# Optimization experiments

Measured on AMD Instinct MI355X. Metric: run time of the kernel, lower is better.

The kernel has to match this reference:

```python
import jax, jax.numpy as jnp
import numpy as np

B, N, D, H = 2, 2048, 1024, 8
HD = D // H  # head_dim = 128
EPS = 1e-6


def setup_inputs() -> dict:
    key = jax.random.key(0)
    ks = jax.random.split(key, 11)
    std = 0.02
    w = lambda k, shape: jax.random.normal(k, shape, dtype=jnp.float32) * std
    return {
        "x": jax.random.normal(ks[0], (B, N, D), dtype=jnp.float32),
        "Wq": w(ks[1], (D, D)),
        "Wk": w(ks[2], (D, D)),
        "Wv": w(ks[3], (D, D)),
        "Wf1": w(ks[4], (D, HD)),
        "Wf2": w(ks[5], (HD, D)),
        "Wbeta": w(ks[6], (D, H)),
        "Wog1": w(ks[7], (D, HD)),
        "Wog2": w(ks[8], (HD, D)),
        "norm_w": jnp.ones((D,), dtype=jnp.float32),
        "Wo": w(ks[9], (D, D)),
    }


def _interleave(a, b):
    # [B,T,H,HD] x2 -> [B,2T,H,HD], order a0,b0,a1,b1,...  (rearrange 'b (c n) -> b (n c)', c=2)
    return jnp.stack([a, b], axis=2).reshape(a.shape[0], 2 * a.shape[1], a.shape[2], a.shape[3])


def _l2norm(x):
    return x / jnp.sqrt(jnp.sum(x * x, axis=-1, keepdims=True) + EPS)


def _dense_rnn(x, Wq, Wk, Wv, Wf1, Wf2, Wbeta, Wog1, Wog2, norm_w, Wo):
    b, n, d = x.shape
    q = jax.nn.silu(x @ Wq)
    k = jax.nn.silu(x @ Wk)
    v = jax.nn.silu(x @ Wv)
    f = (x @ Wf1) @ Wf2                       # low-rank f_proj
    log_f = jax.nn.log_sigmoid(f)
    beta = jax.nn.sigmoid(x @ Wbeta) * 2.0    # [B,N,H], beta_activation='neg'

    shp = (b, n, H, HD)
    q, k, v, log_f = (t.reshape(shp) for t in (q, k, v, log_f))
    k = _l2norm(k)
    k_ = -beta[..., None] * k                 # k * -beta
    zero = jnp.zeros(shp, x.dtype)

    # DPLR doubling: per token, step0 = gated decay + Diag(f)*k k^T, step1 = (I-kk^T)S + k v^T
    gk = _interleave(log_f, zero)
    a = _interleave(k_ * jnp.exp(log_f), k_)
    bb = _interleave(k, k)
    kk = _interleave(zero, k)
    vv = _interleave(zero, v)
    qq = _interleave(zero, q)

    seq = tuple(jnp.moveaxis(t, 1, 0) for t in (gk, a, bb, kk, vv, qq))  # time-major [2N,B,H,HD]
    S0 = jnp.zeros((b, H, HD, HD), x.dtype)

    def step(S, inp):
        g, a_t, b_t, k_t, v_t, q_t = inp
        # S_t = Diag(exp(g)) S + a (b^T S) + k v^T  ; o_t = q^T S_t
        bS = jnp.einsum('bhk,bhkv->bhv', b_t, S)
        S = jnp.exp(g)[..., None] * S + a_t[..., None] * bS[:, :, None, :] + k_t[..., None] * v_t[:, :, None, :]
        o = jnp.einsum('bhk,bhkv->bhv', q_t, S)
        return S, o

    _, o = jax.lax.scan(step, S0, seq)        # o: [2N,B,H,HD]
    o = jnp.moveaxis(o, 0, 1)[:, 1::2]        # take update-step outputs (last n after de-interleave)
    out = o.reshape(b, n, d)

    # gated rmsnorm (gate_pos='pre', sigmoid gate, group = per head) then o_proj
    gate = (x @ Wog1) @ Wog2
    y = out * jax.nn.sigmoid(gate)
    yh = y.reshape(b, n, H, HD)
    yh = yh / jnp.sqrt(jnp.mean(yh * yh, axis=-1, keepdims=True) + EPS)
    y = yh.reshape(b, n, d) * norm_w
    return y @ Wo


def reference(x, Wq, Wk, Wv, Wf1, Wf2, Wbeta, Wog1, Wog2, norm_w, Wo):
    return _dense_rnn(x, Wq, Wk, Wv, Wf1, Wf2, Wbeta, Wog1, Wog2, norm_w, Wo)
```

## Files before the change

### kernel.cpp

```cpp
#include <hip/hip_runtime.h>
#include <cmath>


#define SZT ((size_t)4096 * 1024)
#define RECF 520
#define RECSTRIDE 4160
#define TOKB 16
#define SLOTB 1600

typedef unsigned short u16;
typedef __attribute__((ext_vector_type(8))) short short8;
typedef __attribute__((ext_vector_type(4))) float f32x4;

__device__ __forceinline__ float sigmf(float x) { return 1.f / (1.f + expf(-x)); }
__device__ __forceinline__ float siluf(float x) { return x * sigmf(x); }
__device__ __forceinline__ u16 f2bf(float f) {
    unsigned int u = __float_as_uint(f);
    unsigned int r = (u + 0x7FFFu + ((u >> 16) & 1u)) >> 16;
    return (u16)r;
}
__device__ __forceinline__ float bf2f(u16 h) { return __uint_as_float((unsigned int)h << 16); }
__device__ __forceinline__ void splitbf(float f, u16& hi, u16& lo) {
    hi = f2bf(f);
    lo = f2bf(f - bf2f(hi));
}

#define GLOAD_LDS16(gp, lp) __builtin_amdgcn_global_load_lds( \
    (const __attribute__((address_space(1))) void*)(gp),      \
    (__attribute__((address_space(3))) void*)(lp), 16, 0, 0)

__global__ __launch_bounds__(256) void wtrans_split_g(
    const float* __restrict__ W, u16* __restrict__ WTh, u16* __restrict__ WTl,
    int K, int N)
{
    __shared__ float t[32][33];
    const int tx = threadIdx.x & 31, ty = threadIdx.x >> 5;
    const int n0 = blockIdx.x * 32, k0 = blockIdx.y * 32;
#pragma unroll
    for (int i = 0; i < 4; i++)
        t[ty + i * 8][tx] = W[(size_t)(k0 + ty + i * 8) * N + n0 + tx];
    __syncthreads();
#pragma unroll
    for (int i = 0; i < 4; i++) {
        u16 hi, lo;
        splitbf(t[tx][ty + i * 8], hi, lo);
        WTh[(size_t)(n0 + ty + i * 8) * K + k0 + tx] = hi;
        WTl[(size_t)(n0 + ty + i * 8) * K + k0 + tx] = lo;
    }
}

__global__ __launch_bounds__(256) void wtrans(const float* __restrict__ W, u16* __restrict__ WT)
{
    __shared__ float t[32][33];
    const int tx = threadIdx.x & 31, ty = threadIdx.x >> 5;
    const int n0 = blockIdx.x * 32, k0 = blockIdx.y * 32;
#pragma unroll
    for (int i = 0; i < 4; i++)
        t[ty + i * 8][tx] = W[(size_t)(k0 + ty + i * 8) * 1024 + n0 + tx];
    __syncthreads();
#pragma unroll
    for (int i = 0; i < 4; i++)
        WT[(size_t)(n0 + ty + i * 8) * 1024 + k0 + tx] = f2bf(t[tx][ty + i * 8]);
}

__global__ __launch_bounds__(256) void conv_split(
    const float* __restrict__ in, u16* __restrict__ oh, u16* __restrict__ ol)
{
    const size_t i = ((size_t)blockIdx.x * 256 + threadIdx.x) * 8;
    short8 rh, rl;
#pragma unroll
    for (int j = 0; j < 8; j++) {
        u16 hi, lo;
        splitbf(in[i + j], hi, lo);
        rh[j] = (short)hi; rl[j] = (short)lo;
    }
    *(short8*)&oh[i] = rh;
    *(short8*)&ol[i] = rl;
}

__global__ __launch_bounds__(256) void wcat_kernel(
    const float* __restrict__ Wf1, const float* __restrict__ Wog1, float* __restrict__ Wcat)
{
    const int idx = blockIdx.x * 256 + threadIdx.x;
    const int k = idx >> 8, j = idx & 255;
    Wcat[idx] = (j < 128) ? Wf1[k * 128 + j] : Wog1[k * 128 + j - 128];
}

__global__ __launch_bounds__(256) void beta_kernel(
    const float* __restrict__ x, const float* __restrict__ Wbeta, float* __restrict__ beta)
{
    const int row = blockIdx.x;
    const int tid = threadIdx.x;
    const int lane = tid & 63, wid = tid >> 6;
    __shared__ float wsum[4][8];
    float4 xv = *(const float4*)&x[(size_t)row * 1024 + tid * 4];
    float p[8];
#pragma unroll
    for (int h = 0; h < 8; h++)
        p[h] = xv.x * Wbeta[(size_t)(tid * 4 + 0) * 8 + h]
             + xv.y * Wbeta[(size_t)(tid * 4 + 1) * 8 + h]
             + xv.z * Wbeta[(size_t)(tid * 4 + 2) * 8 + h]
             + xv.w * Wbeta[(size_t)(tid * 4 + 3) * 8 + h];
#pragma unroll
    for (int off = 32; off >= 1; off >>= 1)
#pragma unroll
        for (int h = 0; h < 8; h++) p[h] += __shfl_xor(p[h], off);
    if (lane == 0)
#pragma unroll
        for (int h = 0; h < 8; h++) wsum[wid][h] = p[h];
    __syncthreads();
    if (tid < 8) {
        float s = wsum[0][tid] + wsum[1][tid] + wsum[2][tid] + wsum[3][tid];
        beta[(size_t)row * 8 + tid] = 2.f * sigmf(s);
    }
}

__global__ __launch_bounds__(256) void gemm_bf16_split(
    const u16* __restrict__ Ah, const u16* __restrict__ Al,
    const u16* __restrict__ BTh, const u16* __restrict__ BTl,
    float* __restrict__ C, int M, int N, int K, int lda, int ldb)
{
    __shared__ u16 AsH[128 * 32];
    __shared__ u16 AsL[128 * 32];
    __shared__ u16 BsH[128 * 32];
    __shared__ u16 BsL[128 * 32];
    const int tid = threadIdx.x;
    const int lane = tid & 63;
    const int w = tid >> 6;
    const int wr = w >> 1, wc = w & 1;
    const int row0 = blockIdx.y * 128;
    const int col0 = blockIdx.x * 128;
    const int mrow = lane & 15;
    const int kgrp = (lane >> 4) * 8;

    f32x4 acc[4][4] = {};

    const int off0 = w * 1024 + lane * 16;
    const int r0 = off0 >> 6, kl0 = (off0 & 63) >> 1;
    const int off1 = off0 + 4096;
    const int r1 = off1 >> 6, kl1 = (off1 & 63) >> 1;

    for (int kt = 0; kt < K; kt += 32) {
        GLOAD_LDS16(Ah  + (size_t)(row0 + r0) * lda + kt + kl0, (char*)AsH + w * 1024);
        GLOAD_LDS16(Ah  + (size_t)(row0 + r1) * lda + kt + kl1, (char*)AsH + w * 1024 + 4096);
        GLOAD_LDS16(Al  + (size_t)(row0 + r0) * lda + kt + kl0, (char*)AsL + w * 1024);
        GLOAD_LDS16(Al  + (size_t)(row0 + r1) * lda + kt + kl1, (char*)AsL + w * 1024 + 4096);
        GLOAD_LDS16(BTh + (size_t)(col0 + r0) * ldb + kt + kl0, (char*)BsH + w * 1024);
        GLOAD_LDS16(BTh + (size_t)(col0 + r1) * ldb + kt + kl1, (char*)BsH + w * 1024 + 4096);
        GLOAD_LDS16(BTl + (size_t)(col0 + r0) * ldb + kt + kl0, (char*)BsL + w * 1024);
        GLOAD_LDS16(BTl + (size_t)(col0 + r1) * ldb + kt + kl1, (char*)BsL + w * 1024 + 4096);
        __syncthreads();

        short8 aH[4], aL[4], bH[4], bL[4];
#pragma unroll
        for (int mi = 0; mi < 4; ++mi) {
            aH[mi] = *(const short8*)&AsH[(wr * 64 + mi * 16 + mrow) * 32 + kgrp];
            aL[mi] = *(const short8*)&AsL[(wr * 64 + mi * 16 + mrow) * 32 + kgrp];
        }
#pragma unroll
        for (int ni = 0; ni < 4; ++ni) {
            bH[ni] = *(const short8*)&BsH[(wc * 64 + ni * 16 + mrow) * 32 + kgrp];
            bL[ni] = *(const short8*)&BsL[(wc * 64 + ni * 16 + mrow) * 32 + kgrp];
        }
#pragma unroll
        for (int mi = 0; mi < 4; ++mi)
#pragma unroll
            for (int ni = 0; ni < 4; ++ni) {
                acc[mi][ni] = __builtin_amdgcn_mfma_f32_16x16x32_bf16(aH[mi], bH[ni], acc[mi][ni], 0, 0, 0);
                acc[mi][ni] = __builtin_amdgcn_mfma_f32_16x16x32_bf16(aL[mi], bH[ni], acc[mi][ni], 0, 0, 0);
                acc[mi][ni] = __builtin_amdgcn_mfma_f32_16x16x32_bf16(aH[mi], bL[ni], acc[mi][ni], 0, 0, 0);
            }
        __syncthreads();
    }

    const int crow = (lane >> 4) * 4;
#pragma unroll
    for (int mi = 0; mi < 4; ++mi)
#pragma unroll
        for (int ni = 0; ni < 4; ++ni)
#pragma unroll
            for (int j = 0; j < 4; ++j)
                C[(size_t)(row0 + wr * 64 + mi * 16 + crow + j) * N + col0 + wc * 64 + ni * 16 + mrow]
                    = acc[mi][ni][j];
}

__global__ __launch_bounds__(256) void corr_gemm(
    const u16* __restrict__ Ah, const u16* __restrict__ Al,
    const u16* __restrict__ BTh, const u16* __restrict__ BTl,
    float* __restrict__ OV)
{
    __shared__ u16 AsH[128 * 32];
    __shared__ u16 AsL[128 * 32];
    __shared__ u16 BsH[128 * 32];
    __shared__ u16 BsL[128 * 32];
    const int tid = threadIdx.x;
    const int lane = tid & 63;
    const int w = tid >> 6;
    const int wr = w >> 1, wc = w & 1;
    const int row0 = blockIdx.y * 128;
    const int mrow = lane & 15;
    const int kgrp = (lane >> 4) * 8;

    const int bh = blockIdx.z;
    const int b = bh >> 3, h = bh & 7;
    const size_t aoff = (size_t)b * 2097152 + (size_t)h * 128;
    const size_t boff = (size_t)bh * 16384;
    const size_t coff = (size_t)b * 2097152 + (size_t)1048576 + (size_t)h * 128;

    f32x4 acc[4][4] = {};

    const int off0 = w * 1024 + lane * 16;
    const int r0 = off0 >> 6, kl0 = (off0 & 63) >> 1;
    const int off1 = off0 + 4096;
    const int r1 = off1 >> 6, kl1 = (off1 & 63) >> 1;

    for (int kt = 0; kt < 128; kt += 32) {
        GLOAD_LDS16(Ah  + aoff + (size_t)(row0 + r0) * 1024 + kt + kl0, (char*)AsH + w * 1024);
        GLOAD_LDS16(Ah  + aoff + (size_t)(row0 + r1) * 1024 + kt + kl1, (char*)AsH + w * 1024 + 4096);
        GLOAD_LDS16(Al  + aoff + (size_t)(row0 + r0) * 1024 + kt + kl0, (char*)AsL + w * 1024);
        GLOAD_LDS16(Al  + aoff + (size_t)(row0 + r1) * 1024 + kt + kl1, (char*)AsL + w * 1024 + 4096);
        GLOAD_LDS16(BTh + boff + (size_t)r0 * 128 + kt + kl0, (char*)BsH + w * 1024);
        GLOAD_LDS16(BTh + boff + (size_t)r1 * 128 + kt + kl1, (char*)BsH + w * 1024 + 4096);
        GLOAD_LDS16(BTl + boff + (size_t)r0 * 128 + kt + kl0, (char*)BsL + w * 1024);
        GLOAD_LDS16(BTl + boff + (size_t)r1 * 128 + kt + kl1, (char*)BsL + w * 1024 + 4096);
        __syncthreads();

        short8 aH[4], aL[4], bH[4], bL[4];
#pragma unroll
        for (int mi = 0; mi < 4; ++mi) {
            aH[mi] = *(const short8*)&AsH[(wr * 64 + mi * 16 + mrow) * 32 + kgrp];
            aL[mi] = *(const short8*)&AsL[(wr * 64 + mi * 16 + mrow) * 32 + kgrp];
        }
#pragma unroll
        for (int ni = 0; ni < 4; ++ni) {
            bH[ni] = *(const short8*)&BsH[(wc * 64 + ni * 16 + mrow) * 32 + kgrp];
            bL[ni] = *(const short8*)&BsL[(wc * 64 + ni * 16 + mrow) * 32 + kgrp];
        }
#pragma unroll
        for (int mi = 0; mi < 4; ++mi)
#pragma unroll
            for (int ni = 0; ni < 4; ++ni) {
                acc[mi][ni] = __builtin_amdgcn_mfma_f32_16x16x32_bf16(aH[mi], bH[ni], acc[mi][ni], 0, 0, 0);
                acc[mi][ni] = __builtin_amdgcn_mfma_f32_16x16x32_bf16(aL[mi], bH[ni], acc[mi][ni], 0, 0, 0);
                acc[mi][ni] = __builtin_amdgcn_mfma_f32_16x16x32_bf16(aH[mi], bL[ni], acc[mi][ni], 0, 0, 0);
            }
        __syncthreads();
    }

    const int crow = (lane >> 4) * 4;
#pragma unroll
    for (int mi = 0; mi < 4; ++mi)
#pragma unroll
        for (int ni = 0; ni < 4; ++ni)
#pragma unroll
            for (int j = 0; j < 4; ++j) {
                const size_t idx = coff + (size_t)(row0 + wr * 64 + mi * 16 + crow + j) * 1024
                                 + wc * 64 + ni * 16 + mrow;
                OV[idx] += acc[mi][ni][j];
            }
}

__global__ __launch_bounds__(256) void gemm_bf16(
    const u16* __restrict__ A, const u16* __restrict__ BT, float* __restrict__ C,
    int M, int N, int K)
{
    __shared__ u16 As[128 * 32];
    __shared__ u16 Bs[128 * 32];
    const int tid = threadIdx.x;
    const int lane = tid & 63;
    const int w = tid >> 6;
    const int wr = w >> 1, wc = w & 1;
    const int row0 = blockIdx.y * 128;
    const int col0 = blockIdx.x * 128;
    const int mrow = lane & 15;
    const int kgrp = (lane >> 4) * 8;

    f32x4 acc[4][4] = {};

    const int off0 = w * 1024 + lane * 16;
    const int r0 = off0 >> 6, kl0 = (off0 & 63) >> 1;
    const int off1 = off0 + 4096;
    const int r1 = off1 >> 6, kl1 = (off1 & 63) >> 1;

    for (int kt = 0; kt < K; kt += 32) {
        GLOAD_LDS16(A  + (size_t)(row0 + r0) * K + kt + kl0, (char*)As + w * 1024);
        GLOAD_LDS16(A  + (size_t)(row0 + r1) * K + kt + kl1, (char*)As + w * 1024 + 4096);
        GLOAD_LDS16(BT + (size_t)(col0 + r0) * K + kt + kl0, (char*)Bs + w * 1024);
        GLOAD_LDS16(BT + (size_t)(col0 + r1) * K + kt + kl1, (char*)Bs + w * 1024 + 4096);
        __syncthreads();

        short8 aF[4], bF[4];
#pragma unroll
        for (int mi = 0; mi < 4; ++mi)
            aF[mi] = *(const short8*)&As[(wr * 64 + mi * 16 + mrow) * 32 + kgrp];
#pragma unroll
        for (int ni = 0; ni < 4; ++ni)
            bF[ni] = *(const short8*)&Bs[(wc * 64 + ni * 16 + mrow) * 32 + kgrp];
#pragma unroll
        for (int mi = 0; mi < 4; ++mi)
#pragma unroll
            for (int ni = 0; ni < 4; ++ni)
                acc[mi][ni] = __builtin_amdgcn_mfma_f32_16x16x32_bf16(aF[mi], bF[ni], acc[mi][ni], 0, 0, 0);
        __syncthreads();
    }

    const int crow = (lane >> 4) * 4;
#pragma unroll
    for (int mi = 0; mi < 4; ++mi)
#pragma unroll
        for (int ni = 0; ni < 4; ++ni)
#pragma unroll
            for (int j = 0; j < 4; ++j)
                C[(size_t)(row0 + wr * 64 + mi * 16 + crow + j) * N + col0 + wc * 64 + ni * 16 + mrow]
                    = acc[mi][ni][j];
}

__global__ __launch_bounds__(128) void prep_kernel(
    const float* __restrict__ qkv, const float* __restrict__ fraw,
    const float* __restrict__ beta, float* __restrict__ sb)
{
    const int gid = blockIdx.x;
    const int h = gid & 7;
    const int row = gid >> 3;
    const int tid = threadIdx.x;
    const int col = h * 128 + tid;
    const size_t rb3 = (size_t)row * 3072;

    __shared__ float red[3][128];

    const float ksil = siluf(qkv[rb3 + 1024 + col]);
    red[0][tid] = ksil * ksil;
    __syncthreads();
    for (int off = 64; off > 0; off >>= 1) {
        if (tid < off) red[0][tid] += red[0][tid + off];
        __syncthreads();
    }
    const float rn = rsqrtf(red[0][0] + 1e-6f);
    __syncthreads();

    const float kn = ksil * rn;
    const float e  = sigmf(fraw[(size_t)row * 1024 + col]);
    const float qs = siluf(qkv[rb3 + col]);
    const float vs = siluf(qkv[rb3 + 2048 + col]);
    const float kev = e * kn;
    const float qev = e * qs;

    red[0][tid] = kev * kn;
    red[1][tid] = qs * kev;
    red[2][tid] = qs * kn;
    __syncthreads();
    for (int off = 64; off > 0; off >>= 1) {
        if (tid < off) {
            red[0][tid] += red[0][tid + off];
            red[1][tid] += red[1][tid + off];
            red[2][tid] += red[2][tid + off];
        }
        __syncthreads();
    }

    float* o = sb + (size_t)gid * RECF;
    o[tid]        = kn;
    o[128 + tid]  = e;
    o[256 + tid]  = qev;
    o[384 + tid]  = vs;
    if (tid == 0) {
        o[512] = beta[(size_t)row * 8 + h];
        o[513] = red[0][0];
        o[514] = red[1][0];
        o[515] = red[2][0];
    }
}

__device__ __forceinline__ float red32(float x)
{
    x += __int_as_float(__builtin_amdgcn_mov_dpp(__float_as_int(x), 0xB1,  0xF, 0xF, true));
    x += __int_as_float(__builtin_amdgcn_mov_dpp(__float_as_int(x), 0x4E,  0xF, 0xF, true));
    x += __int_as_float(__builtin_amdgcn_mov_dpp(__float_as_int(x), 0x141, 0xF, 0xF, true));
    x += __int_as_float(__builtin_amdgcn_mov_dpp(__float_as_int(x), 0x140, 0xF, 0xF, true));
    x += __int_as_float(__builtin_amdgcn_ds_swizzle(__float_as_int(x), 0x401F));
    return x;
}

struct TR { float4 k, e, q, sc; float vc; };

__device__ __forceinline__ void ldtok(const char* __restrict__ rec, int rg, int cl, TR& T)
{
    T.k  = *(const float4*)(rec + rg * 16);
    T.e  = *(const float4*)(rec + 512 + rg * 16);
    T.q  = *(const float4*)(rec + 1024 + rg * 16);
    T.vc = *(const float*)(rec + 1536 + cl * 4);
    T.sc = *(const float4*)(rec + 1568);
}

#define STEP(T, SOFF)                                                              \
  {                                                                                \
    const float m0 = T.k.x * S0, m1 = T.k.y * S1, m2 = T.k.z * S2, m3 = T.k.w * S3; \
    float bS  = (m0 + m1) + (m2 + m3);                                             \
    float keS = (T.e.x * m0 + T.e.y * m1) + (T.e.z * m2 + T.e.w * m3);             \
    float qeS = (T.q.x * S0 + T.q.y * S1) + (T.q.z * S2 + T.q.w * S3);             \
    bS = red32(bS); keS = red32(keS); qeS = red32(qeS);                            \
    const float bSb = T.sc.x * bS;                                                 \
    const float ks  = keS - bSb * T.sc.y;                                          \
    const float wv  = T.vc - T.sc.x * ks;                                          \
    const float o   = (qeS - bSb * T.sc.z) + wv * T.sc.w;                          \
    S0 = T.e.x * (S0 - bSb * T.k.x) + wv * T.k.x;                                  \
    S1 = T.e.y * (S1 - bSb * T.k.y) + wv * T.k.y;                                  \
    S2 = T.e.z * (S2 - bSb * T.k.z) + wv * T.k.z;                                  \
    S3 = T.e.w * (S3 - bSb * T.k.w) + wv * T.k.w;                                  \
    if (rg == 0) outp[oidx + (size_t)(SOFF) * 1024] = o;                           \
  }

#define SBAR __builtin_amdgcn_sched_barrier(0)

__device__ __forceinline__ void stage_batch(
    const float* __restrict__ p0, char* ldsbuf, int t0, int w, int lane, int vg)
{
    for (int s = w; s < TOKB; s += 4) {
        const char* src = (const char*)(p0 + (size_t)(t0 + s) * RECSTRIDE);
        char* dst = ldsbuf + s * SLOTB;
        GLOAD_LDS16(src + lane * 16, dst);
        if (lane < 32) GLOAD_LDS16(src + 1024 + lane * 16, dst + 1024);
        if (lane < 2)  GLOAD_LDS16(src + 1536 + vg * 32 + lane * 16, dst + 1536);
        if (lane == 0) GLOAD_LDS16(src + 2048, dst + 1568);
    }
}

__global__ __launch_bounds__(256) void scan_kernel(
    const float* __restrict__ sb, float* __restrict__ ov,
    float* __restrict__ rbuf, float* __restrict__ pbufT)
{
    __shared__ char lds[2 * TOKB * SLOTB];

    const int tid = threadIdx.x;
    const int blk = blockIdx.x;
    const int cl = tid >> 5;
    const int rg = tid & 31;
    const int w = tid >> 6;
    const int lane = tid & 63;

    int bh, vg, tstart, colx;
    bool chunk0, basis = false;
    if (blk < 256) {
        bh = blk & 15; const int cg = blk >> 4;
        colx = cg * 8 + cl; vg = cg; tstart = 0; chunk0 = true;
    } else {
        const int bi = blk - 256;
        bh = bi & 15; const int cg2 = bi >> 4;
        colx = cg2 * 8 + cl; vg = cg2 & 15; tstart = 1024; chunk0 = false;
        basis = colx >= 128;
    }
    const int b = bh >> 3, h = bh & 7;
    const size_t base = (size_t)b * 2048 * 8 + h;
    const float* p0 = sb + base * RECF + (size_t)tstart * RECSTRIDE;

    float* outp;
    size_t oidx;
    if (chunk0)      { outp = ov;   oidx = base * 128 + colx; }
    else if (!basis) { outp = ov;   oidx = base * 128 + (size_t)1048576 + colx; }
    else             { outp = rbuf; oidx = base * 128 + (colx - 128); }

    const float vmask = basis ? 0.f : 1.f;
    float S0, S1, S2, S3;
    if (basis) {
        const int jb = colx - 128;
        S0 = (rg * 4 + 0 == jb) ? 1.f : 0.f;
        S1 = (rg * 4 + 1 == jb) ? 1.f : 0.f;
        S2 = (rg * 4 + 2 == jb) ? 1.f : 0.f;
        S3 = (rg * 4 + 3 == jb) ? 1.f : 0.f;
    } else { S0 = S1 = S2 = S3 = 0.f; }

    stage_batch(p0, lds, 0, w, lane, vg);
    __syncthreads();

    int cur = 0;
    for (int t0 = 0; t0 < 1024; t0 += TOKB) {
        if (t0 + TOKB < 1024)
            stage_batch(p0, lds + (cur ^ 1) * (TOKB * SLOTB), t0 + TOKB, w, lane, vg);

        const char* bufp = lds + cur * (TOKB * SLOTB);
        TR A, B;
        ldtok(bufp, rg, cl, A); A.vc *= vmask; SBAR;
#pragma unroll
        for (int s = 0; s < TOKB; s += 2) {
            ldtok(bufp + (s + 1) * SLOTB, rg, cl, B); B.vc *= vmask; SBAR;
            STEP(A, s);
            if (s + 2 < TOKB) { ldtok(bufp + (s + 2) * SLOTB, rg, cl, A); A.vc *= vmask; SBAR; }
            STEP(B, s + 1);
        }
        __syncthreads();
        cur ^= 1;
        oidx += (size_t)TOKB * 1024;
    }

    if (chunk0) {
        float* pT = pbufT + (size_t)bh * 16384 + (size_t)colx * 128 + rg * 4;
        pT[0] = S0; pT[1] = S1; pT[2] = S2; pT[3] = S3;
    }
}

__global__ __launch_bounds__(128) void post_kernel(
    const float* __restrict__ ov, const float* __restrict__ gate,
    const float* __restrict__ normw, u16* __restrict__ ybf)
{
    const int gid = blockIdx.x;
    const int h = gid & 7;
    const int row = gid >> 3;
    const int tid = threadIdx.x;
    const int col = h * 128 + tid;

    __shared__ float red[128];

    const float o = ov[(size_t)row * 1024 + col];
    const float y = o * sigmf(gate[(size_t)row * 1024 + col]);

    red[tid] = y * y;
    __syncthreads();
    for (int off = 64; off > 0; off >>= 1) {
        if (tid < off) red[tid] += red[tid + off];
        __syncthreads();
    }
    const float rms = rsqrtf(red[0] * (1.f / 128.f) + 1e-6f);
    ybf[(size_t)row * 1024 + col] = f2bf(y * rms * normw[col]);
}

extern "C" void kernel_launch(void* const* d_in, const int* in_sizes, int n_in,
                              void* d_out, int out_size, void* d_ws, size_t ws_size,
                              hipStream_t stream)
{
    const float* x     = (const float*)d_in[0];
    const float* Wq    = (const float*)d_in[1];
    const float* Wk    = (const float*)d_in[2];
    const float* Wv    = (const float*)d_in[3];
    const float* Wf1   = (const float*)d_in[4];
    const float* Wf2   = (const float*)d_in[5];
    const float* Wbeta = (const float*)d_in[6];
    const float* Wog1  = (const float*)d_in[7];
    const float* Wog2  = (const float*)d_in[8];
    const float* normw = (const float*)d_in[9];
    const float* Wo    = (const float*)d_in[10];
    float* out = (float*)d_out;

    float* ws    = (float*)d_ws;
    float* qkv   = ws;
    float* sb    = qkv + 3 * SZT;
    float* ovr   = sb + (size_t)32768 * RECF;
    float* rbuf  = ovr + SZT;
    float* pbufT = rbuf + SZT;
    float* wot   = pbufT + 262144;
    float* wcatT = wot + 524288;
    float* wfog  = wcatT + 262144;
    float* f1sp  = wfog + 262144;
    float* betap = f1sp + 1048576;
    float* psp   = betap + 32768;
    float* xsp   = psp + 262144;

    float* wcat = sb;
    float* f1og = wcat + 262144;

    u16* WqkvTh = (u16*)ovr;
    u16* WqkvTl = WqkvTh + (size_t)3 * 1024 * 1024;
    float* fraw = ovr;

    u16* xh  = (u16*)xsp;
    u16* xl  = xh + SZT;
    u16* rbh = (u16*)xsp;
    u16* rbl = rbh + SZT;

    u16* WoT    = (u16*)wot;
    u16* WcatTh = (u16*)wcatT;
    u16* WcatTl = WcatTh + (size_t)256 * 1024;
    u16* Wf2Th  = (u16*)wfog;
    u16* Wf2Tl  = Wf2Th + (size_t)1024 * 128;
    u16* Wog2Th = Wf2Tl + (size_t)1024 * 128;
    u16* Wog2Tl = Wog2Th + (size_t)1024 * 128;
    u16* f1ogh  = (u16*)f1sp;
    u16* f1ogl  = f1ogh + (size_t)4096 * 256;
    u16* pTh    = (u16*)psp;
    u16* pTl    = pTh + 262144;

    float* gate = qkv;
    u16*   ybf  = (u16*)(qkv + SZT);

    dim3 b256(256), b128(128);

    wtrans_split_g<<<dim3(32, 32), b256, 0, stream>>>(Wq, WqkvTh, WqkvTl, 1024, 1024);
    wtrans_split_g<<<dim3(32, 32), b256, 0, stream>>>(Wk, WqkvTh + (size_t)1024 * 1024, WqkvTl + (size_t)1024 * 1024, 1024, 1024);
    wtrans_split_g<<<dim3(32, 32), b256, 0, stream>>>(Wv, WqkvTh + (size_t)2048 * 1024, WqkvTl + (size_t)2048 * 1024, 1024, 1024);
    wtrans<<<dim3(32, 32), b256, 0, stream>>>(Wo, WoT);
    conv_split<<<2048, b256, 0, stream>>>(x, xh, xl);
    wcat_kernel<<<1024, b256, 0, stream>>>(Wf1, Wog1, wcat);
    wtrans_split_g<<<dim3(8, 32), b256, 0, stream>>>(wcat, WcatTh, WcatTl, 1024, 256);
    wtrans_split_g<<<dim3(32, 4), b256, 0, stream>>>(Wf2, Wf2Th, Wf2Tl, 128, 1024);
    wtrans_split_g<<<dim3(32, 4), b256, 0, stream>>>(Wog2, Wog2Th, Wog2Tl, 128, 1024);
    beta_kernel<<<4096, b256, 0, stream>>>(x, Wbeta, betap);

    gemm_bf16_split<<<dim3(24, 32), b256, 0, stream>>>(xh, xl, WqkvTh, WqkvTl, qkv, 4096, 3072, 1024, 1024, 1024);
    gemm_bf16_split<<<dim3(2, 32), b256, 0, stream>>>(xh, xl, WcatTh, WcatTl, f1og, 4096, 256, 1024, 1024, 1024);
    conv_split<<<512, b256, 0, stream>>>(f1og, f1ogh, f1ogl);
    gemm_bf16_split<<<dim3(8, 32), b256, 0, stream>>>(f1ogh, f1ogl, Wf2Th, Wf2Tl, fraw, 4096, 1024, 128, 256, 128);

    prep_kernel<<<32768, b128, 0, stream>>>(qkv, fraw, betap, sb);
    gemm_bf16_split<<<dim3(8, 32), b256, 0, stream>>>(f1ogh + 128, f1ogl + 128, Wog2Th, Wog2Tl, gate, 4096, 1024, 128, 256, 128);

    scan_kernel<<<768, b256, 0, stream>>>(sb, ovr, rbuf, pbufT);

    conv_split<<<2048, b256, 0, stream>>>(rbuf, rbh, rbl);
    conv_split<<<128, b256, 0, stream>>>(pbufT, pTh, pTl);
    corr_gemm<<<dim3(1, 8, 16), b256, 0, stream>>>(rbh, rbl, pTh, pTl, ovr);

    post_kernel<<<32768, b128, 0, stream>>>(ovr, gate, normw, ybf);

    gemm_bf16<<<dim3(8, 32), b256, 0, stream>>>(ybf, WoT, out, 4096, 1024, 1024);
}
```

Measured before the change: 728.4 us.

## Halve scan threads per column and fuse bf16 split into scan outputs

The scan kernel now gives each thread 8 state rows instead of 4, so a column is handled by 16 lanes instead of 32. This cuts the cross-lane reduction from 5 stages to 4 and halves the block size. The prep kernel permutes the k/e/q record layout to match the new split-float4 loads. The scan also writes the basis outputs and final states directly as hi/lo bf16 pairs, which removes two conv_split launches and their fp32 round trip through memory. The trade-offs are more register pressure and fewer threads per block for latency hiding on this serial recurrence.

```diff
diff --git a/kernel.cpp b/kernel.cpp
--- a/kernel.cpp
+++ b/kernel.cpp
@@ -358,11 +358,12 @@
         __syncthreads();
     }
 
+    const int p = ((tid & 4) << 4) + ((tid >> 3) << 2) + (tid & 3);
     float* o = sb + (size_t)gid * RECF;
-    o[tid]        = kn;
-    o[128 + tid]  = e;
-    o[256 + tid]  = qev;
-    o[384 + tid]  = vs;
+    o[p]         = kn;
+    o[128 + p]   = e;
+    o[256 + p]   = qev;
+    o[384 + tid] = vs;
     if (tid == 0) {
         o[512] = beta[(size_t)row * 8 + h];
         o[513] = red[0][0];
@@ -371,43 +372,60 @@
     }
 }
 
-__device__ __forceinline__ float red32(float x)
+__device__ __forceinline__ float red16(float x)
 {
     x += __int_as_float(__builtin_amdgcn_mov_dpp(__float_as_int(x), 0xB1,  0xF, 0xF, true));
     x += __int_as_float(__builtin_amdgcn_mov_dpp(__float_as_int(x), 0x4E,  0xF, 0xF, true));
     x += __int_as_float(__builtin_amdgcn_mov_dpp(__float_as_int(x), 0x141, 0xF, 0xF, true));
     x += __int_as_float(__builtin_amdgcn_mov_dpp(__float_as_int(x), 0x140, 0xF, 0xF, true));
-    x += __int_as_float(__builtin_amdgcn_ds_swizzle(__float_as_int(x), 0x401F));
     return x;
 }
 
-struct TR { float4 k, e, q, sc; float vc; };
+struct TR { float4 ka, kb, ea, eb, qa, qb, sc; float vc; };
 
 __device__ __forceinline__ void ldtok(const char* __restrict__ rec, int rg, int cl, TR& T)
 {
-    T.k  = *(const float4*)(rec + rg * 16);
-    T.e  = *(const float4*)(rec + 512 + rg * 16);
-    T.q  = *(const float4*)(rec + 1024 + rg * 16);
+    T.ka = *(const float4*)(rec + rg * 16);
+    T.kb = *(const float4*)(rec + 256 + rg * 16);
+    T.ea = *(const float4*)(rec + 512 + rg * 16);
+    T.eb = *(const float4*)(rec + 768 + rg * 16);
+    T.qa = *(const float4*)(rec + 1024 + rg * 16);
+    T.qb = *(const float4*)(rec + 1280 + rg * 16);
     T.vc = *(const float*)(rec + 1536 + cl * 4);
     T.sc = *(const float4*)(rec + 1568);
 }
 
-#define STEP(T, SOFF)                                                              \
-  {                                                                                \
-    const float m0 = T.k.x * S0, m1 = T.k.y * S1, m2 = T.k.z * S2, m3 = T.k.w * S3; \
-    float bS  = (m0 + m1) + (m2 + m3);                                             \
-    float keS = (T.e.x * m0 + T.e.y * m1) + (T.e.z * m2 + T.e.w * m3);             \
-    float qeS = (T.q.x * S0 + T.q.y * S1) + (T.q.z * S2 + T.q.w * S3);             \
-    bS = red32(bS); keS = red32(keS); qeS = red32(qeS);                            \
-    const float bSb = T.sc.x * bS;                                                 \
-    const float ks  = keS - bSb * T.sc.y;                                          \
-    const float wv  = T.vc - T.sc.x * ks;                                          \
-    const float o   = (qeS - bSb * T.sc.z) + wv * T.sc.w;                          \
-    S0 = T.e.x * (S0 - bSb * T.k.x) + wv * T.k.x;                                  \
-    S1 = T.e.y * (S1 - bSb * T.k.y) + wv * T.k.y;                                  \
-    S2 = T.e.z * (S2 - bSb * T.k.z) + wv * T.k.z;                                  \
-    S3 = T.e.w * (S3 - bSb * T.k.w) + wv * T.k.w;                                  \
-    if (rg == 0) outp[oidx + (size_t)(SOFF) * 1024] = o;                           \
+#define STEP(T, SOFF)                                                                   \
+  {                                                                                     \
+    const float m0 = T.ka.x * S0, m1 = T.ka.y * S1, m2 = T.ka.z * S2, m3 = T.ka.w * S3; \
+    const float m4 = T.kb.x * S4, m5 = T.kb.y * S5, m6 = T.kb.z * S6, m7 = T.kb.w * S7; \
+    float bS  = ((m0 + m1) + (m2 + m3)) + ((m4 + m5) + (m6 + m7));                      \
+    float keS = ((T.ea.x * m0 + T.ea.y * m1) + (T.ea.z * m2 + T.ea.w * m3))             \
+              + ((T.eb.x * m4 + T.eb.y * m5) + (T.eb.z * m6 + T.eb.w * m7));            \
+    float qeS = ((T.qa.x * S0 + T.qa.y * S1) + (T.qa.z * S2 + T.qa.w * S3))             \
+              + ((T.qb.x * S4 + T.qb.y * S5) + (T.qb.z * S6 + T.qb.w * S7));            \
+    bS = red16(bS); keS = red16(keS); qeS = red16(qeS);                                 \
+    const float bSb = T.sc.x * bS;                                                      \
+    const float ks  = keS - bSb * T.sc.y;                                               \
+    const float wv  = T.vc - T.sc.x * ks;                                               \
+    const float o   = (qeS - bSb * T.sc.z) + wv * T.sc.w;                               \
+    S0 = T.ea.x * (S0 - bSb * T.ka.x) + wv * T.ka.x;                                    \
+    S1 = T.ea.y * (S1 - bSb * T.ka.y) + wv * T.ka.y;                                    \
+    S2 = T.ea.z * (S2 - bSb * T.ka.z) + wv * T.ka.z;                                    \
+    S3 = T.ea.w * (S3 - bSb * T.ka.w) + wv * T.ka.w;                                    \
+    S4 = T.eb.x * (S4 - bSb * T.kb.x) + wv * T.kb.x;                                    \
+    S5 = T.eb.y * (S5 - bSb * T.kb.y) + wv * T.kb.y;                                    \
+    S6 = T.eb.z * (S6 - bSb * T.kb.z) + wv * T.kb.z;                                    \
+    S7 = T.eb.w * (S7 - bSb * T.kb.w) + wv * T.kb.w;                                    \
+    if (rg == 0) {                                                                      \
+        if (basis) {                                                                    \
+            u16 hi, lo; splitbf(o, hi, lo);                                             \
+            rbh[oidx + (size_t)(SOFF) * 1024] = hi;                                     \
+            rbl[oidx + (size_t)(SOFF) * 1024] = lo;                                     \
+        } else {                                                                        \
+            ov[oidx + (size_t)(SOFF) * 1024] = o;                                       \
+        }                                                                               \
+    }                                                                                   \
   }
 
 #define SBAR __builtin_amdgcn_sched_barrier(0)
@@ -415,7 +433,7 @@
 __device__ __forceinline__ void stage_batch(
     const float* __restrict__ p0, char* ldsbuf, int t0, int w, int lane, int vg)
 {
-    for (int s = w; s < TOKB; s += 4) {
+    for (int s = w; s < TOKB; s += 2) {
         const char* src = (const char*)(p0 + (size_t)(t0 + s) * RECSTRIDE);
         char* dst = ldsbuf + s * SLOTB;
         GLOAD_LDS16(src + lane * 16, dst);
@@ -425,27 +443,29 @@
     }
 }
 
-__global__ __launch_bounds__(256) void scan_kernel(
+__global__ __launch_bounds__(128) void scan_kernel(
     const float* __restrict__ sb, float* __restrict__ ov,
-    float* __restrict__ rbuf, float* __restrict__ pbufT)
+    u16* __restrict__ rbh, u16* __restrict__ rbl,
+    u16* __restrict__ pTh, u16* __restrict__ pTl)
 {
     __shared__ char lds[2 * TOKB * SLOTB];
 
     const int tid = threadIdx.x;
     const int blk = blockIdx.x;
-    const int cl = tid >> 5;
-    const int rg = tid & 31;
+    const int cl = tid >> 4;
+    const int rg = tid & 15;
     const int w = tid >> 6;
     const int lane = tid & 63;
 
-    int bh, vg, tstart, colx;
+    const int bh = blk & 15;
+    const int gidx = blk >> 4;
+
+    int vg, tstart, colx;
     bool chunk0, basis = false;
-    if (blk < 256) {
-        bh = blk & 15; const int cg = blk >> 4;
-        colx = cg * 8 + cl; vg = cg; tstart = 0; chunk0 = true;
+    if (gidx < 16) {
+        colx = gidx * 8 + cl; vg = gidx; tstart = 0; chunk0 = true;
     } else {
-        const int bi = blk - 256;
-        bh = bi & 15; const int cg2 = bi >> 4;
+        const int cg2 = gidx - 16;
         colx = cg2 * 8 + cl; vg = cg2 & 15; tstart = 1024; chunk0 = false;
         basis = colx >= 128;
     }
@@ -453,21 +473,24 @@
     const size_t base = (size_t)b * 2048 * 8 + h;
     const float* p0 = sb + base * RECF + (size_t)tstart * RECSTRIDE;
 
-    float* outp;
     size_t oidx;
-    if (chunk0)      { outp = ov;   oidx = base * 128 + colx; }
-    else if (!basis) { outp = ov;   oidx = base * 128 + (size_t)1048576 + colx; }
-    else             { outp = rbuf; oidx = base * 128 + (colx - 128); }
+    if (chunk0)      oidx = base * 128 + colx;
+    else if (!basis) oidx = base * 128 + (size_t)1048576 + colx;
+    else             oidx = base * 128 + (colx - 128);
 
     const float vmask = basis ? 0.f : 1.f;
-    float S0, S1, S2, S3;
+    float S0, S1, S2, S3, S4, S5, S6, S7;
     if (basis) {
         const int jb = colx - 128;
-        S0 = (rg * 4 + 0 == jb) ? 1.f : 0.f;
-        S1 = (rg * 4 + 1 == jb) ? 1.f : 0.f;
-        S2 = (rg * 4 + 2 == jb) ? 1.f : 0.f;
-        S3 = (rg * 4 + 3 == jb) ? 1.f : 0.f;
-    } else { S0 = S1 = S2 = S3 = 0.f; }
+        S0 = (rg * 8 + 0 == jb) ? 1.f : 0.f;
+        S1 = (rg * 8 + 1 == jb) ? 1.f : 0.f;
+        S2 = (rg * 8 + 2 == jb) ? 1.f : 0.f;
+        S3 = (rg * 8 + 3 == jb) ? 1.f : 0.f;
+        S4 = (rg * 8 + 4 == jb) ? 1.f : 0.f;
+        S5 = (rg * 8 + 5 == jb) ? 1.f : 0.f;
+        S6 = (rg * 8 + 6 == jb) ? 1.f : 0.f;
+        S7 = (rg * 8 + 7 == jb) ? 1.f : 0.f;
+    } else { S0 = S1 = S2 = S3 = S4 = S5 = S6 = S7 = 0.f; }
 
     stage_batch(p0, lds, 0, w, lane, vg);
     __syncthreads();
@@ -493,8 +516,16 @@
     }
 
     if (chunk0) {
-        float* pT = pbufT + (size_t)bh * 16384 + (size_t)colx * 128 + rg * 4;
-        pT[0] = S0; pT[1] = S1; pT[2] = S2; pT[3] = S3;
+        float Sv[8] = {S0, S1, S2, S3, S4, S5, S6, S7};
+        short8 h8, l8;
+#pragma unroll
+        for (int i = 0; i < 8; i++) {
+            u16 hi, lo; splitbf(Sv[i], hi, lo);
+            h8[i] = (short)hi; l8[i] = (short)lo;
+        }
+        const size_t po = (size_t)bh * 16384 + (size_t)colx * 128 + rg * 8;
+        *(short8*)(pTh + po) = h8;
+        *(short8*)(pTl + po) = l8;
     }
 }
 
@@ -544,15 +575,14 @@
     float* qkv   = ws;
     float* sb    = qkv + 3 * SZT;
     float* ovr   = sb + (size_t)32768 * RECF;
-    float* rbuf  = ovr + SZT;
-    float* pbufT = rbuf + SZT;
-    float* wot   = pbufT + 262144;
+    float* rbspace = ovr + SZT;
+    float* pbspace = rbspace + SZT;
+    float* wot   = pbspace + 262144;
     float* wcatT = wot + 524288;
     float* wfog  = wcatT + 262144;
     float* f1sp  = wfog + 262144;
     float* betap = f1sp + 1048576;
-    float* psp   = betap + 32768;
-    float* xsp   = psp + 262144;
+    float* xsp   = betap + 32768;
 
     float* wcat = sb;
     float* f1og = wcat + 262144;
@@ -563,8 +593,11 @@
 
     u16* xh  = (u16*)xsp;
     u16* xl  = xh + SZT;
-    u16* rbh = (u16*)xsp;
+
+    u16* rbh = (u16*)rbspace;
     u16* rbl = rbh + SZT;
+    u16* pTh = (u16*)pbspace;
+    u16* pTl = pTh + 262144;
 
     u16* WoT    = (u16*)wot;
     u16* WcatTh = (u16*)wcatT;
@@ -575,8 +608,6 @@
     u16* Wog2Tl = Wog2Th + (size_t)1024 * 128;
     u16* f1ogh  = (u16*)f1sp;
     u16* f1ogl  = f1ogh + (size_t)4096 * 256;
-    u16* pTh    = (u16*)psp;
-    u16* pTl    = pTh + 262144;
 
     float* gate = qkv;
     u16*   ybf  = (u16*)(qkv + SZT);
@@ -602,10 +633,8 @@
     prep_kernel<<<32768, b128, 0, stream>>>(qkv, fraw, betap, sb);
     gemm_bf16_split<<<dim3(8, 32), b256, 0, stream>>>(f1ogh + 128, f1ogl + 128, Wog2Th, Wog2Tl, gate, 4096, 1024, 128, 256, 128);
 
-    scan_kernel<<<768, b256, 0, stream>>>(sb, ovr, rbuf, pbufT);
-
-    conv_split<<<2048, b256, 0, stream>>>(rbuf, rbh, rbl);
-    conv_split<<<128, b256, 0, stream>>>(pbufT, pTh, pTl);
+    scan_kernel<<<768, b128, 0, stream>>>(sb, ovr, rbh, rbl, pTh, pTl);
+
     corr_gemm<<<dim3(1, 8, 16), b256, 0, stream>>>(rbh, rbl, pTh, pTl, ovr);
 
     post_kernel<<<32768, b128, 0, stream>>>(ovr, gate, normw, ybf);
```

Result: slower. 772.3 us (+6.0%).
